# Kernel tuning notes

Measured on AMD Instinct MI355X. Metric: run time of the kernel, lower is better.

## Reference

```python
import jax, jax.numpy as jnp
import numpy as np

CONV_DIMS = (-3, -2)   # spatial dims (channel-last layout)
RADIUS = (3, 3)        # window = 1 + 2*r = 7 per dim -> 49 cells
STEP = (1, 1)


def _unfold(x, dim, window, step):
    """torch.Tensor.unfold: dim -> out_len, window appended as last axis."""
    dim = dim % x.ndim
    n = x.shape[dim]
    starts = jnp.arange((n - window) // step + 1) * step          # [L]
    idx = starts[:, None] + jnp.arange(window)[None, :]           # [L, w]
    y = jnp.take(x, idx, axis=dim)                                # dim -> [L, w]
    return jnp.moveaxis(y, dim + 1, -1)                           # window axis to last


def _local_attention(x):
    # Unfold each conv dim; move its window axis to the front (as in the torch code).
    for i, r, s in zip(CONV_DIMS, RADIUS, STEP):
        x = _unfold(x, i, 1 + 2 * r, s)
        x = jnp.moveaxis(x, -1, 0)
    n_win = len(CONV_DIMS)
    cells = int(np.prod(x.shape[:n_win]))
    x = x.reshape((cells,) + x.shape[n_win:])      # [cells, B, H', W', C]
    center = cells // 2                            # spatial center of the window
    q = jnp.moveaxis(x[center:center + 1], 0, -2)  # [B, H', W', 1, C]
    k = jnp.moveaxis(jnp.concatenate([x[:center], x[center + 1:]], axis=0), 0, -2)  # [B,H',W',cells-1,C]
    d = q.shape[-1]
    scores = jnp.einsum('...qc,...kc->...qk', q, k) / jnp.sqrt(jnp.asarray(d, q.dtype))
    w = jax.nn.softmax(scores, axis=-1)
    out = jnp.einsum('...qk,...kc->...qc', w, k)   # keys double as values
    return out.squeeze(-2)                          # [B, H', W', C]


def setup_inputs() -> dict:
    key = jax.random.key(0)
    X = jax.random.normal(key, (4, 64, 64, 256), dtype=jnp.float32)
    return {"X": X}


def reference(X):
    return _local_attention(X)
```

## Files before the change

### kernel.cpp

```cpp
#include <hip/hip_runtime.h>

#define B_   4
#define H_   64
#define W_   64
#define C_   256
#define HO_  58
#define WO_  58
#define TI_  29
#define TJ_  8
#define GRID (B_ * TI_ * TJ_)

typedef __attribute__((ext_vector_type(8))) short bf16x8;
typedef __attribute__((ext_vector_type(4))) float f32x4;

__device__ __forceinline__ void split2(float a, float b, unsigned& hi, unsigned& lo) {
    unsigned ua = __builtin_bit_cast(unsigned, a);
    unsigned ub = __builtin_bit_cast(unsigned, b);
    hi = (ua >> 16) | (ub & 0xFFFF0000u);
    float ra = a - __builtin_bit_cast(float, ua & 0xFFFF0000u);
    float rb = b - __builtin_bit_cast(float, ub & 0xFFFF0000u);
    lo = (__builtin_bit_cast(unsigned, ra) >> 16) |
         (__builtin_bit_cast(unsigned, rb) & 0xFFFF0000u);
}

__device__ __forceinline__ void split8(const float* v, bf16x8& h, bf16x8& l) {
    uint4 hu, lu;
    split2(v[0], v[1], hu.x, lu.x);
    split2(v[2], v[3], hu.y, lu.y);
    split2(v[4], v[5], hu.z, lu.z);
    split2(v[6], v[7], hu.w, lu.w);
    h = __builtin_bit_cast(bf16x8, hu);
    l = __builtin_bit_cast(bf16x8, lu);
}

__device__ __forceinline__ bf16x8 ldfrag(const short* arr, int row, int col, int rowBytes) {
    int byte = (row * rowBytes + col * 2) ^ ((row & 7) << 4);
    return *(const bf16x8*)((const char*)arr + byte);
}

__global__ __launch_bounds__(256, 3) void convnd_attn_kernel(const float* __restrict__ X,
                                                             float* __restrict__ out) {
    __shared__ __align__(16) float Spart[4][128][16];
    __shared__ __align__(16) short Wh[16 * 128];
    __shared__ __align__(16) short Wl[16 * 128];
    __shared__ float psum[16][16];
    __shared__ float rtot[16];

    const int sp  = (blockIdx.x & 7) * 116 + (blockIdx.x >> 3);
    const int tj  = sp & 7;
    const int rst = sp >> 3;
    const int ti  = rst % TI_;
    const int b   = rst / TI_;
    const int i0  = ti * 2;
    const int j0  = (tj < 7) ? tj * 8 : 50;

    const int tid  = threadIdx.x;
    const int wave = tid >> 6;
    const int lane = tid & 63;
    const int lr   = lane & 15;
    const int g    = lane >> 4;
    const int kb8  = g << 3;

    const float* base = X + (size_t)b * (H_ * W_ * C_);

    bf16x8 qh[2], ql[2];
    {
        const int aq = lr >> 3, bq = lr & 7;
        const float* qp = base + (((i0 + aq + 3) * W_) + (j0 + bq + 3)) * C_
                        + wave * 64 + kb8;
        #pragma unroll
        for (int ks = 0; ks < 2; ++ks) {
            float v[8];
            float4 x0 = *(const float4*)(qp + ks * 32);
            float4 x1 = *(const float4*)(qp + ks * 32 + 4);
            v[0]=x0.x*0.0625f; v[1]=x0.y*0.0625f; v[2]=x0.z*0.0625f; v[3]=x0.w*0.0625f;
            v[4]=x1.x*0.0625f; v[5]=x1.y*0.0625f; v[6]=x1.z*0.0625f; v[7]=x1.w*0.0625f;
            split8(v, qh[ks], ql[ks]);
        }
    }

    f32x4 accS[8];
    #pragma unroll
    for (int t = 0; t < 8; ++t) accS[t] = (f32x4){0.f, 0.f, 0.f, 0.f};

    const int dj13 = (lr < 13) ? lr : 13;
    const float* up0 = base + (j0 + dj13) * C_ + wave * 64 + kb8;
    #pragma unroll
    for (int t = 0; t < 8; ++t) {
        const float* ur = up0 + (size_t)(i0 + t) * (W_ * C_);
        #pragma unroll
        for (int ks = 0; ks < 2; ++ks) {
            float v[8];
            float4 x0 = *(const float4*)(ur + ks * 32);
            float4 x1 = *(const float4*)(ur + ks * 32 + 4);
            v[0]=x0.x; v[1]=x0.y; v[2]=x0.z; v[3]=x0.w;
            v[4]=x1.x; v[5]=x1.y; v[6]=x1.z; v[7]=x1.w;
            bf16x8 uh, ul;
            split8(v, uh, ul);
            accS[t] = __builtin_amdgcn_mfma_f32_16x16x32_bf16(uh, qh[ks], accS[t], 0, 0, 0);
            accS[t] = __builtin_amdgcn_mfma_f32_16x16x32_bf16(uh, ql[ks], accS[t], 0, 0, 0);
            accS[t] = __builtin_amdgcn_mfma_f32_16x16x32_bf16(ul, qh[ks], accS[t], 0, 0, 0);
        }
    }
    #pragma unroll
    for (int t = 0; t < 8; ++t) {
        #pragma unroll
        for (int rr = 0; rr < 4; ++rr)
            Spart[wave][t * 16 + g * 4 + rr][lr] = accS[t][rr];
    }
    __syncthreads();

    const int spx = tid & 15, seg = tid >> 4;
    {
        const int sa = spx >> 3, sb = spx & 7;
        float e[8]; float ps = 0.f;
        #pragma unroll
        for (int k = 0; k < 8; ++k) {
            const int cell = seg * 8 + k;
            const int di = (cell >> 4) - sa, dj = (cell & 15) - sb;
            const bool valid = (di >= 0) & (di <= 6) & (dj >= 0) & (dj <= 6)
                               & !((di == 3) & (dj == 3));
            const float s = Spart[0][cell][spx] + Spart[1][cell][spx]
                          + Spart[2][cell][spx] + Spart[3][cell][spx];
            e[k] = valid ? __expf(s) : 0.f;
            ps += e[k];
        }
        psum[seg][spx] = ps;
        __syncthreads();
        if (tid < 16) {
            float t2 = 0.f;
            #pragma unroll
            for (int s2 = 0; s2 < 16; ++s2) t2 += psum[s2][tid];
            rtot[tid] = 1.0f / t2;
        }
        __syncthreads();
        const float rt = rtot[spx];
        unsigned h0,h1,h2,h3, l0,l1,l2,l3;
        split2(e[0]*rt, e[1]*rt, h0, l0);
        split2(e[2]*rt, e[3]*rt, h1, l1);
        split2(e[4]*rt, e[5]*rt, h2, l2);
        split2(e[6]*rt, e[7]*rt, h3, l3);
        const int wb = (spx * 256 + seg * 16) ^ ((spx & 7) << 4);
        *(uint4*)((char*)Wh + wb) = make_uint4(h0, h1, h2, h3);
        *(uint4*)((char*)Wl + wb) = make_uint4(l0, l1, l2, l3);
    }
    __syncthreads();

    bf16x8 wfh[4], wfl[4];
    #pragma unroll
    for (int ks = 0; ks < 4; ++ks) {
        wfh[ks] = ldfrag(Wh, lr, ks * 32 + kb8, 256);
        wfl[ks] = ldfrag(Wl, lr, ks * 32 + kb8, 256);
    }

    #pragma unroll
    for (int cc = 0; cc < 4; ++cc) {
        const int ch = (wave * 4 + cc) * 16 + lr;
        f32x4 accO = {0.f, 0.f, 0.f, 0.f};
        #pragma unroll
        for (int ks = 0; ks < 4; ++ks) {
            const int di  = ks * 2 + (g >> 1);
            const int dj0 = (g & 1) * 8;
            const float* vb = base + (((i0 + di) * W_) + j0) * C_ + ch;
            float v[8];
            #pragma unroll
            for (int e2 = 0; e2 < 8; ++e2) {
                const int dj = (dj0 + e2 < 13) ? dj0 + e2 : 13;
                v[e2] = vb[dj * C_];
            }
            bf16x8 vh, vl;
            split8(v, vh, vl);
            accO = __builtin_amdgcn_mfma_f32_16x16x32_bf16(wfh[ks], vh, accO, 0, 0, 0);
            accO = __builtin_amdgcn_mfma_f32_16x16x32_bf16(wfh[ks], vl, accO, 0, 0, 0);
            accO = __builtin_amdgcn_mfma_f32_16x16x32_bf16(wfl[ks], vh, accO, 0, 0, 0);
        }
        #pragma unroll
        for (int rr = 0; rr < 4; ++rr) {
            const int px = g * 4 + rr;
            const int aa = px >> 3, bb = px & 7;
            out[(((size_t)b * HO_ + (i0 + aa)) * WO_ + (j0 + bb)) * C_ + ch] = accO[rr];
        }
    }
}

extern "C" void kernel_launch(void* const* d_in, const int* in_sizes, int n_in,
                              void* d_out, int out_size, void* d_ws, size_t ws_size,
                              hipStream_t stream) {
    const float* X = (const float*)d_in[0];
    float* outp    = (float*)d_out;
    hipLaunchKernelGGL(convnd_attn_kernel,
                       dim3(GRID), dim3(256), 0, stream, X, outp);
}
```

Baseline: 91.64 us.

## Use hardware bf16 pack conversion, alias shared memory, and software-pipeline global loads

Replaces the manual bit-mask bf16 hi/lo split with the v_cvt_pk_bf16_f32 instruction, which rounds instead of truncating. Shared memory is aliased so the weight buffers reuse the score buffer, which shrinks the LDS footprint and lets launch bounds request 4 blocks per SM. Both MFMA loops (QK and weights times V) are flattened and double-buffered, so the next global loads are in flight while the current fragment is converted and multiplied. This trades more live registers under the tighter occupancy bound for better latency hiding, and risks spills.

```diff
diff --git a/kernel.cpp b/kernel.cpp
--- a/kernel.cpp
+++ b/kernel.cpp
@@ -13,22 +13,22 @@
 typedef __attribute__((ext_vector_type(8))) short bf16x8;
 typedef __attribute__((ext_vector_type(4))) float f32x4;
 
-__device__ __forceinline__ void split2(float a, float b, unsigned& hi, unsigned& lo) {
-    unsigned ua = __builtin_bit_cast(unsigned, a);
-    unsigned ub = __builtin_bit_cast(unsigned, b);
-    hi = (ua >> 16) | (ub & 0xFFFF0000u);
-    float ra = a - __builtin_bit_cast(float, ua & 0xFFFF0000u);
-    float rb = b - __builtin_bit_cast(float, ub & 0xFFFF0000u);
-    lo = (__builtin_bit_cast(unsigned, ra) >> 16) |
-         (__builtin_bit_cast(unsigned, rb) & 0xFFFF0000u);
-}
-
-__device__ __forceinline__ void split8(const float* v, bf16x8& h, bf16x8& l) {
+__device__ __forceinline__ unsigned cvtpk(float a, float b) {
+    unsigned r;
+    asm("v_cvt_pk_bf16_f32 %0, %1, %2" : "=v"(r) : "v"(a), "v"(b));
+    return r;
+}
+__device__ __forceinline__ float lo16f(unsigned h) { return __builtin_bit_cast(float, h << 16); }
+__device__ __forceinline__ float hi16f(unsigned h) { return __builtin_bit_cast(float, h & 0xFFFF0000u); }
+
+__device__ __forceinline__ void split8cvt(const float* v, bf16x8& h, bf16x8& l) {
     uint4 hu, lu;
-    split2(v[0], v[1], hu.x, lu.x);
-    split2(v[2], v[3], hu.y, lu.y);
-    split2(v[4], v[5], hu.z, lu.z);
-    split2(v[6], v[7], hu.w, lu.w);
+    hu.x = cvtpk(v[0], v[1]); hu.y = cvtpk(v[2], v[3]);
+    hu.z = cvtpk(v[4], v[5]); hu.w = cvtpk(v[6], v[7]);
+    lu.x = cvtpk(v[0] - lo16f(hu.x), v[1] - hi16f(hu.x));
+    lu.y = cvtpk(v[2] - lo16f(hu.y), v[3] - hi16f(hu.y));
+    lu.z = cvtpk(v[4] - lo16f(hu.z), v[5] - hi16f(hu.z));
+    lu.w = cvtpk(v[6] - lo16f(hu.w), v[7] - hi16f(hu.w));
     h = __builtin_bit_cast(bf16x8, hu);
     l = __builtin_bit_cast(bf16x8, lu);
 }
@@ -38,13 +38,14 @@
     return *(const bf16x8*)((const char*)arr + byte);
 }
 
-__global__ __launch_bounds__(256, 3) void convnd_attn_kernel(const float* __restrict__ X,
+__global__ __launch_bounds__(256, 4) void convnd_attn_kernel(const float* __restrict__ X,
                                                              float* __restrict__ out) {
-    __shared__ __align__(16) float Spart[4][128][16];
-    __shared__ __align__(16) short Wh[16 * 128];
-    __shared__ __align__(16) short Wl[16 * 128];
-    __shared__ float psum[16][16];
-    __shared__ float rtot[16];
+    __shared__ __align__(16) char smem[32768 + 1024 + 64];
+    float (*Spart)[128][16] = reinterpret_cast<float (*)[128][16]>(smem);
+    short* Wh = reinterpret_cast<short*>(smem);
+    short* Wl = reinterpret_cast<short*>(smem + 4096);
+    float (*psum)[16] = reinterpret_cast<float (*)[16]>(smem + 32768);
+    float* rtot = reinterpret_cast<float*>(smem + 32768 + 1024);
 
     const int sp  = (blockIdx.x & 7) * 116 + (blockIdx.x >> 3);
     const int tj  = sp & 7;
@@ -70,12 +71,11 @@
                         + wave * 64 + kb8;
         #pragma unroll
         for (int ks = 0; ks < 2; ++ks) {
-            float v[8];
             float4 x0 = *(const float4*)(qp + ks * 32);
             float4 x1 = *(const float4*)(qp + ks * 32 + 4);
-            v[0]=x0.x*0.0625f; v[1]=x0.y*0.0625f; v[2]=x0.z*0.0625f; v[3]=x0.w*0.0625f;
-            v[4]=x1.x*0.0625f; v[5]=x1.y*0.0625f; v[6]=x1.z*0.0625f; v[7]=x1.w*0.0625f;
-            split8(v, qh[ks], ql[ks]);
+            float v[8] = {x0.x*0.0625f, x0.y*0.0625f, x0.z*0.0625f, x0.w*0.0625f,
+                          x1.x*0.0625f, x1.y*0.0625f, x1.z*0.0625f, x1.w*0.0625f};
+            split8cvt(v, qh[ks], ql[ks]);
         }
     }
 
@@ -84,23 +84,30 @@
     for (int t = 0; t < 8; ++t) accS[t] = (f32x4){0.f, 0.f, 0.f, 0.f};
 
     const int dj13 = (lr < 13) ? lr : 13;
-    const float* up0 = base + (j0 + dj13) * C_ + wave * 64 + kb8;
-    #pragma unroll
-    for (int t = 0; t < 8; ++t) {
-        const float* ur = up0 + (size_t)(i0 + t) * (W_ * C_);
-        #pragma unroll
-        for (int ks = 0; ks < 2; ++ks) {
-            float v[8];
-            float4 x0 = *(const float4*)(ur + ks * 32);
-            float4 x1 = *(const float4*)(ur + ks * 32 + 4);
-            v[0]=x0.x; v[1]=x0.y; v[2]=x0.z; v[3]=x0.w;
-            v[4]=x1.x; v[5]=x1.y; v[6]=x1.z; v[7]=x1.w;
-            bf16x8 uh, ul;
-            split8(v, uh, ul);
-            accS[t] = __builtin_amdgcn_mfma_f32_16x16x32_bf16(uh, qh[ks], accS[t], 0, 0, 0);
-            accS[t] = __builtin_amdgcn_mfma_f32_16x16x32_bf16(uh, ql[ks], accS[t], 0, 0, 0);
-            accS[t] = __builtin_amdgcn_mfma_f32_16x16x32_bf16(ul, qh[ks], accS[t], 0, 0, 0);
-        }
+    const float* up0 = base + (size_t)i0 * (W_ * C_) + (j0 + dj13) * C_ + wave * 64 + kb8;
+
+    float4 pfa[2], pfb[2];
+    pfa[0] = *(const float4*)(up0);
+    pfb[0] = *(const float4*)(up0 + 4);
+    pfa[1] = *(const float4*)(up0 + 32);
+    pfb[1] = *(const float4*)(up0 + 36);
+    #pragma unroll
+    for (int it = 0; it < 16; ++it) {
+        const int t = it >> 1;
+        float v[8];
+        { float4 c0 = pfa[it & 1], c1 = pfb[it & 1];
+          v[0]=c0.x; v[1]=c0.y; v[2]=c0.z; v[3]=c0.w;
+          v[4]=c1.x; v[5]=c1.y; v[6]=c1.z; v[7]=c1.w; }
+        if (it + 2 < 16) {
+            const float* p = up0 + ((it + 2) >> 1) * (W_ * C_) + ((it + 2) & 1) * 32;
+            pfa[it & 1] = *(const float4*)(p);
+            pfb[it & 1] = *(const float4*)(p + 4);
+        }
+        bf16x8 uh, ul;
+        split8cvt(v, uh, ul);
+        accS[t] = __builtin_amdgcn_mfma_f32_16x16x32_bf16(uh, qh[it & 1], accS[t], 0, 0, 0);
+        accS[t] = __builtin_amdgcn_mfma_f32_16x16x32_bf16(uh, ql[it & 1], accS[t], 0, 0, 0);
+        accS[t] = __builtin_amdgcn_mfma_f32_16x16x32_bf16(ul, qh[it & 1], accS[t], 0, 0, 0);
     }
     #pragma unroll
     for (int t = 0; t < 8; ++t) {
@@ -135,14 +142,19 @@
         }
         __syncthreads();
         const float rt = rtot[spx];
-        unsigned h0,h1,h2,h3, l0,l1,l2,l3;
-        split2(e[0]*rt, e[1]*rt, h0, l0);
-        split2(e[2]*rt, e[3]*rt, h1, l1);
-        split2(e[4]*rt, e[5]*rt, h2, l2);
-        split2(e[6]*rt, e[7]*rt, h3, l3);
+        uint4 hu, lu;
+        float w0, w1;
+        w0 = e[0]*rt; w1 = e[1]*rt; hu.x = cvtpk(w0, w1);
+        lu.x = cvtpk(w0 - lo16f(hu.x), w1 - hi16f(hu.x));
+        w0 = e[2]*rt; w1 = e[3]*rt; hu.y = cvtpk(w0, w1);
+        lu.y = cvtpk(w0 - lo16f(hu.y), w1 - hi16f(hu.y));
+        w0 = e[4]*rt; w1 = e[5]*rt; hu.z = cvtpk(w0, w1);
+        lu.z = cvtpk(w0 - lo16f(hu.z), w1 - hi16f(hu.z));
+        w0 = e[6]*rt; w1 = e[7]*rt; hu.w = cvtpk(w0, w1);
+        lu.w = cvtpk(w0 - lo16f(hu.w), w1 - hi16f(hu.w));
         const int wb = (spx * 256 + seg * 16) ^ ((spx & 7) << 4);
-        *(uint4*)((char*)Wh + wb) = make_uint4(h0, h1, h2, h3);
-        *(uint4*)((char*)Wl + wb) = make_uint4(l0, l1, l2, l3);
+        *(uint4*)((char*)Wh + wb) = make_uint4(hu.x, hu.y, hu.z, hu.w);
+        *(uint4*)((char*)Wl + wb) = make_uint4(lu.x, lu.y, lu.z, lu.w);
     }
     __syncthreads();
 
@@ -153,32 +165,54 @@
         wfl[ks] = ldfrag(Wl, lr, ks * 32 + kb8, 256);
     }
 
+    int voff[8];
+    {
+        const int dj0 = (g & 1) * 8;
+        #pragma unroll
+        for (int e2 = 0; e2 < 8; ++e2) {
+            int dj = dj0 + e2; if (dj > 13) dj = 13;
+            voff[e2] = (g >> 1) * (W_ * C_) + dj * C_;
+        }
+    }
+    const float* vbase = base + (size_t)i0 * (W_ * C_) + j0 * C_ + wave * 64 + lr;
+
+    f32x4 accO[4];
+    #pragma unroll
+    for (int cc = 0; cc < 4; ++cc) accO[cc] = (f32x4){0.f, 0.f, 0.f, 0.f};
+
+    float pv[2][8];
+    #pragma unroll
+    for (int e2 = 0; e2 < 8; ++e2) pv[0][e2] = vbase[voff[e2]];
+    #pragma unroll
+    for (int e2 = 0; e2 < 8; ++e2) pv[1][e2] = (vbase + 16)[voff[e2]];
+
+    #pragma unroll
+    for (int it = 0; it < 16; ++it) {
+        const int ks = it >> 2, cc = it & 3;
+        float v[8];
+        #pragma unroll
+        for (int e2 = 0; e2 < 8; ++e2) v[e2] = pv[it & 1][e2];
+        if (it + 2 < 16) {
+            const int ks2 = (it + 2) >> 2, cc2 = (it + 2) & 3;
+            const float* p = vbase + (size_t)(ks2 * 2) * (W_ * C_) + cc2 * 16;
+            #pragma unroll
+            for (int e2 = 0; e2 < 8; ++e2) pv[it & 1][e2] = p[voff[e2]];
+        }
+        bf16x8 vh, vl;
+        split8cvt(v, vh, vl);
+        accO[cc] = __builtin_amdgcn_mfma_f32_16x16x32_bf16(wfh[ks], vh, accO[cc], 0, 0, 0);
+        accO[cc] = __builtin_amdgcn_mfma_f32_16x16x32_bf16(wfh[ks], vl, accO[cc], 0, 0, 0);
+        accO[cc] = __builtin_amdgcn_mfma_f32_16x16x32_bf16(wfl[ks], vh, accO[cc], 0, 0, 0);
+    }
+
     #pragma unroll
     for (int cc = 0; cc < 4; ++cc) {
         const int ch = (wave * 4 + cc) * 16 + lr;
-        f32x4 accO = {0.f, 0.f, 0.f, 0.f};
-        #pragma unroll
-        for (int ks = 0; ks < 4; ++ks) {
-            const int di  = ks * 2 + (g >> 1);
-            const int dj0 = (g & 1) * 8;
-            const float* vb = base + (((i0 + di) * W_) + j0) * C_ + ch;
-            float v[8];
-            #pragma unroll
-            for (int e2 = 0; e2 < 8; ++e2) {
-                const int dj = (dj0 + e2 < 13) ? dj0 + e2 : 13;
-                v[e2] = vb[dj * C_];
-            }
-            bf16x8 vh, vl;
-            split8(v, vh, vl);
-            accO = __builtin_amdgcn_mfma_f32_16x16x32_bf16(wfh[ks], vh, accO, 0, 0, 0);
-            accO = __builtin_amdgcn_mfma_f32_16x16x32_bf16(wfh[ks], vl, accO, 0, 0, 0);
-            accO = __builtin_amdgcn_mfma_f32_16x16x32_bf16(wfl[ks], vh, accO, 0, 0, 0);
-        }
         #pragma unroll
         for (int rr = 0; rr < 4; ++rr) {
             const int px = g * 4 + rr;
             const int aa = px >> 3, bb = px & 7;
-            out[(((size_t)b * HO_ + (i0 + aa)) * WO_ + (j0 + bb)) * C_ + ch] = accO[rr];
+            out[(((size_t)b * HO_ + (i0 + aa)) * WO_ + (j0 + bb)) * C_ + ch] = accO[cc][rr];
         }
     }
 }
```

Result: faster. 87.77 us (-4.2%).
